# Kernel optimization log

Measured on AMD Instinct MI355X. Metric: run time of the kernel, lower is better.

The kernel has to match this reference:

```python
import jax, jax.numpy as jnp
import numpy as np

N, E, D_IN, D_OUT = 50000, 800000, 128, 64


def setup_inputs() -> dict:
    key = jax.random.key(0)
    ks = jax.random.split(key, 8)
    s = 1.0 / np.sqrt(D_IN)
    return {
        "x": jax.random.normal(ks[0], (N, D_IN), jnp.float32),
        "edge_index": jax.random.randint(ks[1], (2, E), 0, N),
        "edge_weight": jax.random.uniform(ks[2], (E,), jnp.float32),
        "init_w": jax.random.normal(ks[3], (D_IN, D_IN), jnp.float32) * s,
        "gru_w_ih": jax.random.normal(ks[4], (3 * D_IN, D_IN), jnp.float32) * s,
        "gru_w_hh": jax.random.normal(ks[5], (3 * D_IN, D_IN), jnp.float32) * s,
        "gru_b_ih": jnp.zeros((3 * D_IN,), jnp.float32),
        "gru_b_hh": jnp.zeros((3 * D_IN,), jnp.float32),
        "lin_w": jax.random.normal(ks[6], (D_OUT, D_IN), jnp.float32) * s,
        "lin_b": jnp.zeros((D_OUT,), jnp.float32),
    }


def _gru_step(x, h, w_ih, w_hh, b_ih, b_hh):
    # torch GRU gate order: r, z, n
    gi = x @ w_ih.T + b_ih
    gh = h @ w_hh.T + b_hh
    i_r, i_z, i_n = jnp.split(gi, 3, axis=-1)
    h_r, h_z, h_n = jnp.split(gh, 3, axis=-1)
    r = jax.nn.sigmoid(i_r + h_r)
    z = jax.nn.sigmoid(i_z + h_z)
    n = jnp.tanh(i_n + r * h_n)
    return (1.0 - z) * n + z * h


def reference(x, edge_index, edge_weight, init_w, gru_w_ih, gru_w_hh, gru_b_ih, gru_b_hh, lin_w, lin_b):
    n_nodes = x.shape[0]
    # EvolveGCNO: evolve W via one GRU step, W is both input and hidden (rows = GRU batch)
    W = _gru_step(init_w, init_w, gru_w_ih, gru_w_hh, gru_b_ih, gru_b_hh)  # [D_IN, D_IN]

    # gcn_norm with self-loops (fill value 1.0)
    loop = jnp.arange(n_nodes)
    row = jnp.concatenate([edge_index[0], loop])  # source j
    col = jnp.concatenate([edge_index[1], loop])  # target i
    w = jnp.concatenate([edge_weight, jnp.ones((n_nodes,), x.dtype)])
    deg = jax.ops.segment_sum(w, col, num_segments=n_nodes)
    dis = jnp.where(deg > 0, jax.lax.rsqrt(jnp.maximum(deg, 1e-12)), 0.0)
    norm = dis[row] * w * dis[col]  # [E+N]

    xw = x @ W  # [N, D_IN]
    h = jax.ops.segment_sum(norm[:, None] * xw[row], col, num_segments=n_nodes)
    h = jax.nn.relu(h)
    return h @ lin_w.T + lin_b  # [N, D_OUT]
```

## Files before the change

### kernel.cpp

```cpp
#include <hip/hip_runtime.h>
#include <hip/hip_fp16.h>
#include <math.h>

#define NN 50000
#define NE 800000
#define D  128
#define D3 384
#define DO 64
#define NPAD 50048
#define NSH 4

typedef _Float16 f16x2 __attribute__((ext_vector_type(2)));

__device__ __forceinline__ float dot2acc(unsigned int h2bits, unsigned int wbits,
                                         float acc) {
#if __has_builtin(__builtin_amdgcn_fdot2)
  return __builtin_amdgcn_fdot2(__builtin_bit_cast(f16x2, h2bits),
                                __builtin_bit_cast(f16x2, wbits), acc, false);
#else
  float2 hf = __half22float2(__builtin_bit_cast(__half2, h2bits));
  float2 wf = __half22float2(__builtin_bit_cast(__half2, wbits));
  return acc + hf.x * wf.x + hf.y * wf.y;
#endif
}

__device__ __forceinline__ unsigned int pk_f16(float a, float b) {
#if __has_builtin(__builtin_amdgcn_cvt_pkrtz)
  return __builtin_bit_cast(unsigned int, __builtin_amdgcn_cvt_pkrtz(a, b));
#else
  return __builtin_bit_cast(unsigned int, __floats2half2_rn(a, b));
#endif
}

__global__ __launch_bounds__(256) void setup_kernel(
    const float* __restrict__ init_w, const float* __restrict__ w_ih,
    const float* __restrict__ w_hh, const float* __restrict__ b_ih,
    const float* __restrict__ b_hh, __half* __restrict__ Wh,
    unsigned long long* __restrict__ packed4, int* __restrict__ total) {
  if (blockIdx.x >= 64) {
    int i = (blockIdx.x - 64) * 256 + threadIdx.x;
    if (i < NSH * NPAD) packed4[i] = 0ULL;
    if (i == 0) *total = 0;
    return;
  }
  int idx = blockIdx.x * 256 + threadIdx.x;
  int b = idx >> 7;
  int j = idx & 127;
  const float* xr = init_w + b * D;
  const float* wr_i = w_ih + j * D;
  const float* wz_i = w_ih + (D + j) * D;
  const float* wn_i = w_ih + (2 * D + j) * D;
  const float* wr_h = w_hh + j * D;
  const float* wz_h = w_hh + (D + j) * D;
  const float* wn_h = w_hh + (2 * D + j) * D;
  float ir = 0.f, iz = 0.f, in_ = 0.f, hr = 0.f, hz = 0.f, hn = 0.f;
#pragma unroll 4
  for (int k = 0; k < D; ++k) {
    float xv = xr[k];
    ir += xv * wr_i[k];
    iz += xv * wz_i[k];
    in_ += xv * wn_i[k];
    hr += xv * wr_h[k];
    hz += xv * wz_h[k];
    hn += xv * wn_h[k];
  }
  ir += b_ih[j];       hr += b_hh[j];
  iz += b_ih[D + j];   hz += b_hh[D + j];
  in_ += b_ih[2 * D + j]; hn += b_hh[2 * D + j];
  float r = 1.f / (1.f + expf(-(ir + hr)));
  float z = 1.f / (1.f + expf(-(iz + hz)));
  float n = tanhf(in_ + r * hn);
  Wh[idx] = (__half)((1.f - z) * n + z * init_w[idx]);
}

__global__ __launch_bounds__(256) void count_deg_kernel(const int* __restrict__ col,
                                                        const float* __restrict__ ew,
                                                        unsigned long long* __restrict__ packed4,
                                                        int* __restrict__ rank) {
  int e = blockIdx.x * 256 + threadIdx.x;
  if (e < NE) {
    int s = blockIdx.x & (NSH - 1);
    int c = __builtin_nontemporal_load(&col[e]);
    float w = __builtin_nontemporal_load(&ew[e]);
    unsigned long long add = (1ULL << 40) | (unsigned long long)(w * 4294967296.0f);
    unsigned long long old = atomicAdd(&packed4[s * NPAD + c], add);
    __builtin_nontemporal_store((s << 28) | (int)(old >> 40), &rank[e]);
  }
}

__global__ __launch_bounds__(256) void dis_scan_kernel(
    const unsigned long long* __restrict__ packed4, float* __restrict__ dis,
    int* __restrict__ cnt, unsigned int* __restrict__ start4,
    int* __restrict__ total) {
  const unsigned long long M = (1ULL << 40) - 1;
  int i = blockIdx.x * 256 + threadIdx.x;
  int lane = threadIdx.x & 63;
  int c0 = 0, c1 = 0, c2 = 0, c3 = 0;
  float d = 1.0f;
  if (i < NN) {
    unsigned long long p0 = packed4[i];
    unsigned long long p1 = packed4[NPAD + i];
    unsigned long long p2 = packed4[2 * NPAD + i];
    unsigned long long p3 = packed4[3 * NPAD + i];
    c0 = (int)(p0 >> 40);
    c1 = (int)(p1 >> 40);
    c2 = (int)(p2 >> 40);
    c3 = (int)(p3 >> 40);
    unsigned long long dsum = (p0 & M) + (p1 & M) + (p2 & M) + (p3 & M);
    d += (float)dsum * 0x1p-32f;
  }
  int c = c0 + c1 + c2 + c3;
  int cp = (c + 3) & ~3;
  int pre = cp;
#pragma unroll
  for (int off = 1; off < 64; off <<= 1) {
    int t = __shfl_up(pre, off, 64);
    if (lane >= off) pre += t;
  }
  int excl = pre - cp;
  int wtot = __shfl(pre, 63, 64);
  int base = 0;
  if (lane == 63) base = atomicAdd(total, wtot);
  base = __shfl(base, 63, 64);
  if (i < NN) {
    unsigned int st = base + excl;
    start4[i] = st;
    start4[NPAD + i] = st + c0;
    start4[2 * NPAD + i] = st + c0 + c1;
    start4[3 * NPAD + i] = st + c0 + c1 + c2;
    cnt[i] = c;
    dis[i] = rsqrtf(fmaxf(d, 1e-12f));
  }
}

__global__ __launch_bounds__(256) void bucket_kernel(
    const int* __restrict__ row, const int* __restrict__ col,
    const float* __restrict__ ew, const int* __restrict__ rank,
    const float* __restrict__ dis, const unsigned int* __restrict__ start4,
    unsigned int* __restrict__ epack) {
  int e = blockIdx.x * 256 + threadIdx.x;
  if (e >= NE) return;
  int j = __builtin_nontemporal_load(&row[e]);
  int c = __builtin_nontemporal_load(&col[e]);
  float w = __builtin_nontemporal_load(&ew[e]);
  int rk = __builtin_nontemporal_load(&rank[e]);
  int s = rk >> 28;
  int r = rk & 0x0fffffff;
  float nrm = dis[j] * w * dis[c];
  unsigned short wb = __builtin_bit_cast(unsigned short, (_Float16)nrm);
  int slot = start4[s * NPAD + c] + r;
  __builtin_nontemporal_store((unsigned int)j | ((unsigned int)wb << 16),
                              &epack[slot]);
}

__global__ __launch_bounds__(256) void xw_kernel(const float* __restrict__ x,
                                                 const __half* __restrict__ Wh,
                                                 __half* __restrict__ xwh) {
  __shared__ unsigned int U[64 * 128];
  {
    const unsigned short* Wu = (const unsigned short*)Wh;
    for (int i = threadIdx.x; i < 64 * 128; i += 256) {
      int kp = i >> 7, c = i & 127;
      unsigned int lo = Wu[(2 * kp) * D + c];
      unsigned int hi = Wu[(2 * kp + 1) * D + c];
      int sl = (c >> 3) + ((c & 4) ? 16 : 0);
      U[kp * 128 + sl * 4 + (c & 3)] = lo | (hi << 16);
    }
  }
  __syncthreads();
  const int t = threadIdx.x;
  const int rr = t >> 4;
  const int ci = t & 15;
  const uint4* U4 = (const uint4*)U;
  for (int base = blockIdx.x * 32; base < NN; base += gridDim.x * 32) {
    float acc[2][8];
#pragma unroll
    for (int q = 0; q < 2; ++q)
#pragma unroll
      for (int j = 0; j < 8; ++j) acc[q][j] = 0.f;
    const int r0 = base + rr;
    const int r1 = r0 + 16;
    const bool v0 = r0 < NN, v1 = r1 < NN;
    const float* xp0 = x + (long)r0 * D;
    const float* xp1 = x + (long)r1 * D;
#pragma unroll 2
    for (int k0 = 0; k0 < D; k0 += 4) {
      float4 xa = v0 ? *(const float4*)(xp0 + k0) : make_float4(0.f, 0.f, 0.f, 0.f);
      float4 xb = v1 ? *(const float4*)(xp1 + k0) : make_float4(0.f, 0.f, 0.f, 0.f);
      unsigned int xa0 = pk_f16(xa.x, xa.y), xa1 = pk_f16(xa.z, xa.w);
      unsigned int xb0 = pk_f16(xb.x, xb.y), xb1 = pk_f16(xb.z, xb.w);
      int kp = k0 >> 1;
      uint4 wA = U4[kp * 32 + ci];
      uint4 wB = U4[kp * 32 + ci + 16];
      uint4 wC = U4[(kp + 1) * 32 + ci];
      uint4 wD = U4[(kp + 1) * 32 + ci + 16];
      acc[0][0] = dot2acc(xa0, wA.x, acc[0][0]);
      acc[0][1] = dot2acc(xa0, wA.y, acc[0][1]);
      acc[0][2] = dot2acc(xa0, wA.z, acc[0][2]);
      acc[0][3] = dot2acc(xa0, wA.w, acc[0][3]);
      acc[0][4] = dot2acc(xa0, wB.x, acc[0][4]);
      acc[0][5] = dot2acc(xa0, wB.y, acc[0][5]);
      acc[0][6] = dot2acc(xa0, wB.z, acc[0][6]);
      acc[0][7] = dot2acc(xa0, wB.w, acc[0][7]);
      acc[1][0] = dot2acc(xb0, wA.x, acc[1][0]);
      acc[1][1] = dot2acc(xb0, wA.y, acc[1][1]);
      acc[1][2] = dot2acc(xb0, wA.z, acc[1][2]);
      acc[1][3] = dot2acc(xb0, wA.w, acc[1][3]);
      acc[1][4] = dot2acc(xb0, wB.x, acc[1][4]);
      acc[1][5] = dot2acc(xb0, wB.y, acc[1][5]);
      acc[1][6] = dot2acc(xb0, wB.z, acc[1][6]);
      acc[1][7] = dot2acc(xb0, wB.w, acc[1][7]);
      acc[0][0] = dot2acc(xa1, wC.x, acc[0][0]);
      acc[0][1] = dot2acc(xa1, wC.y, acc[0][1]);
      acc[0][2] = dot2acc(xa1, wC.z, acc[0][2]);
      acc[0][3] = dot2acc(xa1, wC.w, acc[0][3]);
      acc[0][4] = dot2acc(xa1, wD.x, acc[0][4]);
      acc[0][5] = dot2acc(xa1, wD.y, acc[0][5]);
      acc[0][6] = dot2acc(xa1, wD.z, acc[0][6]);
      acc[0][7] = dot2acc(xa1, wD.w, acc[0][7]);
      acc[1][0] = dot2acc(xb1, wC.x, acc[1][0]);
      acc[1][1] = dot2acc(xb1, wC.y, acc[1][1]);
      acc[1][2] = dot2acc(xb1, wC.z, acc[1][2]);
      acc[1][3] = dot2acc(xb1, wC.w, acc[1][3]);
      acc[1][4] = dot2acc(xb1, wD.x, acc[1][4]);
      acc[1][5] = dot2acc(xb1, wD.y, acc[1][5]);
      acc[1][6] = dot2acc(xb1, wD.z, acc[1][6]);
      acc[1][7] = dot2acc(xb1, wD.w, acc[1][7]);
    }
#pragma unroll
    for (int q = 0; q < 2; ++q) {
      int r = r0 + q * 16;
      if (r < NN) {
        unsigned int pk[4];
#pragma unroll
        for (int j = 0; j < 4; ++j)
          pk[j] = __builtin_bit_cast(
              unsigned int, __floats2half2_rn(acc[q][2 * j], acc[q][2 * j + 1]));
        *(uint4*)(xwh + (long)r * D + ci * 8) = *(uint4*)pk;
      }
    }
  }
}

__global__ __launch_bounds__(256) void gather_out_kernel(
    const unsigned int* __restrict__ start4, const int* __restrict__ cnt,
    const unsigned int* __restrict__ epack, const float* __restrict__ dis,
    const __half* __restrict__ xwh, const float* __restrict__ lin_w,
    const float* __restrict__ lin_b, float* __restrict__ out) {
  __shared__ unsigned int LTh[64 * 64];
  __shared__ unsigned int hb[4][2][64];
  for (int idx = threadIdx.x; idx < 64 * 64; idx += 256) {
    int kk = idx >> 6, o = idx & 63;
    __half2 w2 = __floats2half2_rn(lin_w[o * D + 2 * kk], lin_w[o * D + 2 * kk + 1]);
    LTh[idx] = __builtin_bit_cast(unsigned int, w2);
  }
  __syncthreads();
  const int wv = threadIdx.x >> 6;
  const int lane = threadIdx.x & 63;
  const float bias = lin_b[lane];
  const __half2* __restrict__ yw2 = (const __half2*)xwh;
  int gw = blockIdx.x * 4 + wv;
  int nw = gridDim.x * 4;
  for (int i = gw; i < NN; i += 2 * nw) {
    const int iB = i + nw;
    const bool hasB = iB < NN;
    float dsA = dis[i], dsA2 = dsA * dsA;
    float2 svA = __half22float2(yw2[(long)i * 64 + lane]);
    float aA0 = dsA2 * svA.x, aA1 = dsA2 * svA.y;
    float aB0 = 0.f, aB1 = 0.f;
    int sA = start4[i], seA = sA + cnt[i];
    int sB = 0, seB = 0;
    if (hasB) {
      float dsB = dis[iB], dsB2 = dsB * dsB;
      float2 svB = __half22float2(yw2[(long)iB * 64 + lane]);
      aB0 = dsB2 * svB.x;
      aB1 = dsB2 * svB.y;
      sB = start4[iB];
      seB = sB + cnt[iB];
    }
    while (sA + 4 <= seA && sB + 4 <= seB) {
      uint4 pA = *(const uint4*)(epack + sA);
      uint4 pB = *(const uint4*)(epack + sB);
      __half2 vA0 = yw2[(long)(pA.x & 0xffff) * 64 + lane];
      __half2 vA1 = yw2[(long)(pA.y & 0xffff) * 64 + lane];
      __half2 vA2 = yw2[(long)(pA.z & 0xffff) * 64 + lane];
      __half2 vA3 = yw2[(long)(pA.w & 0xffff) * 64 + lane];
      __half2 vB0 = yw2[(long)(pB.x & 0xffff) * 64 + lane];
      __half2 vB1 = yw2[(long)(pB.y & 0xffff) * 64 + lane];
      __half2 vB2 = yw2[(long)(pB.z & 0xffff) * 64 + lane];
      __half2 vB3 = yw2[(long)(pB.w & 0xffff) * 64 + lane];
      _Float16 wA0 = __builtin_bit_cast(_Float16, (unsigned short)(pA.x >> 16));
      _Float16 wA1 = __builtin_bit_cast(_Float16, (unsigned short)(pA.y >> 16));
      _Float16 wA2 = __builtin_bit_cast(_Float16, (unsigned short)(pA.z >> 16));
      _Float16 wA3 = __builtin_bit_cast(_Float16, (unsigned short)(pA.w >> 16));
      _Float16 wB0 = __builtin_bit_cast(_Float16, (unsigned short)(pB.x >> 16));
      _Float16 wB1 = __builtin_bit_cast(_Float16, (unsigned short)(pB.y >> 16));
      _Float16 wB2 = __builtin_bit_cast(_Float16, (unsigned short)(pB.z >> 16));
      _Float16 wB3 = __builtin_bit_cast(_Float16, (unsigned short)(pB.w >> 16));
      aA0 += (float)wA0 * (float)__low2half(vA0) + (float)wA1 * (float)__low2half(vA1) +
             (float)wA2 * (float)__low2half(vA2) + (float)wA3 * (float)__low2half(vA3);
      aA1 += (float)wA0 * (float)__high2half(vA0) + (float)wA1 * (float)__high2half(vA1) +
             (float)wA2 * (float)__high2half(vA2) + (float)wA3 * (float)__high2half(vA3);
      aB0 += (float)wB0 * (float)__low2half(vB0) + (float)wB1 * (float)__low2half(vB1) +
             (float)wB2 * (float)__low2half(vB2) + (float)wB3 * (float)__low2half(vB3);
      aB1 += (float)wB0 * (float)__high2half(vB0) + (float)wB1 * (float)__high2half(vB1) +
             (float)wB2 * (float)__high2half(vB2) + (float)wB3 * (float)__high2half(vB3);
      sA += 4;
      sB += 4;
    }
    for (; sA + 4 <= seA; sA += 4) {
      uint4 p = *(const uint4*)(epack + sA);
      __half2 v0 = yw2[(long)(p.x & 0xffff) * 64 + lane];
      __half2 v1 = yw2[(long)(p.y & 0xffff) * 64 + lane];
      __half2 v2 = yw2[(long)(p.z & 0xffff) * 64 + lane];
      __half2 v3 = yw2[(long)(p.w & 0xffff) * 64 + lane];
      _Float16 w0 = __builtin_bit_cast(_Float16, (unsigned short)(p.x >> 16));
      _Float16 w1 = __builtin_bit_cast(_Float16, (unsigned short)(p.y >> 16));
      _Float16 w2 = __builtin_bit_cast(_Float16, (unsigned short)(p.z >> 16));
      _Float16 w3 = __builtin_bit_cast(_Float16, (unsigned short)(p.w >> 16));
      aA0 += (float)w0 * (float)__low2half(v0) + (float)w1 * (float)__low2half(v1) +
             (float)w2 * (float)__low2half(v2) + (float)w3 * (float)__low2half(v3);
      aA1 += (float)w0 * (float)__high2half(v0) + (float)w1 * (float)__high2half(v1) +
             (float)w2 * (float)__high2half(v2) + (float)w3 * (float)__high2half(v3);
    }
    for (; sA < seA; ++sA) {
      unsigned int p = epack[sA];
      _Float16 w0 = __builtin_bit_cast(_Float16, (unsigned short)(p >> 16));
      __half2 v0 = yw2[(long)(p & 0xffff) * 64 + lane];
      aA0 += (float)w0 * (float)__low2half(v0);
      aA1 += (float)w0 * (float)__high2half(v0);
    }
    for (; sB + 4 <= seB; sB += 4) {
      uint4 p = *(const uint4*)(epack + sB);
      __half2 v0 = yw2[(long)(p.x & 0xffff) * 64 + lane];
      __half2 v1 = yw2[(long)(p.y & 0xffff) * 64 + lane];
      __half2 v2 = yw2[(long)(p.z & 0xffff) * 64 + lane];
      __half2 v3 = yw2[(long)(p.w & 0xffff) * 64 + lane];
      _Float16 w0 = __builtin_bit_cast(_Float16, (unsigned short)(p.x >> 16));
      _Float16 w1 = __builtin_bit_cast(_Float16, (unsigned short)(p.y >> 16));
      _Float16 w2 = __builtin_bit_cast(_Float16, (unsigned short)(p.z >> 16));
      _Float16 w3 = __builtin_bit_cast(_Float16, (unsigned short)(p.w >> 16));
      aB0 += (float)w0 * (float)__low2half(v0) + (float)w1 * (float)__low2half(v1) +
             (float)w2 * (float)__low2half(v2) + (float)w3 * (float)__low2half(v3);
      aB1 += (float)w0 * (float)__high2half(v0) + (float)w1 * (float)__high2half(v1) +
             (float)w2 * (float)__high2half(v2) + (float)w3 * (float)__high2half(v3);
    }
    for (; sB < seB; ++sB) {
      unsigned int p = epack[sB];
      _Float16 w0 = __builtin_bit_cast(_Float16, (unsigned short)(p >> 16));
      __half2 v0 = yw2[(long)(p & 0xffff) * 64 + lane];
      aB0 += (float)w0 * (float)__low2half(v0);
      aB1 += (float)w0 * (float)__high2half(v0);
    }
    hb[wv][0][lane] = __builtin_bit_cast(
        unsigned int, __floats2half2_rn(fmaxf(aA0, 0.f), fmaxf(aA1, 0.f)));
    if (hasB) {
      hb[wv][1][lane] = __builtin_bit_cast(
          unsigned int, __floats2half2_rn(fmaxf(aB0, 0.f), fmaxf(aB1, 0.f)));
    }
    asm volatile("s_waitcnt lgkmcnt(0)" ::: "memory");
    {
      float ac0 = bias, ac1 = 0.f, ac2 = 0.f, ac3 = 0.f;
      const uint4* hrow = (const uint4*)&hb[wv][0][0];
#pragma unroll
      for (int c = 0; c < 16; ++c) {
        uint4 v = hrow[c];
        ac0 = dot2acc(v.x, LTh[(4 * c + 0) * 64 + lane], ac0);
        ac1 = dot2acc(v.y, LTh[(4 * c + 1) * 64 + lane], ac1);
        ac2 = dot2acc(v.z, LTh[(4 * c + 2) * 64 + lane], ac2);
        ac3 = dot2acc(v.w, LTh[(4 * c + 3) * 64 + lane], ac3);
      }
      __builtin_nontemporal_store((ac0 + ac1) + (ac2 + ac3),
                                  &out[(long)i * DO + lane]);
    }
    if (hasB) {
      float ac0 = bias, ac1 = 0.f, ac2 = 0.f, ac3 = 0.f;
      const uint4* hrow = (const uint4*)&hb[wv][1][0];
#pragma unroll
      for (int c = 0; c < 16; ++c) {
        uint4 v = hrow[c];
        ac0 = dot2acc(v.x, LTh[(4 * c + 0) * 64 + lane], ac0);
        ac1 = dot2acc(v.y, LTh[(4 * c + 1) * 64 + lane], ac1);
        ac2 = dot2acc(v.z, LTh[(4 * c + 2) * 64 + lane], ac2);
        ac3 = dot2acc(v.w, LTh[(4 * c + 3) * 64 + lane], ac3);
      }
      __builtin_nontemporal_store((ac0 + ac1) + (ac2 + ac3),
                                  &out[(long)iB * DO + lane]);
    }
    asm volatile("s_waitcnt lgkmcnt(0)" ::: "memory");
  }
}

extern "C" void kernel_launch(void* const* d_in, const int* in_sizes, int n_in,
                              void* d_out, int out_size, void* d_ws, size_t ws_size,
                              hipStream_t stream) {
  const float* x      = (const float*)d_in[0];
  const int*   eidx   = (const int*)d_in[1];
  const float* ew     = (const float*)d_in[2];
  const float* init_w = (const float*)d_in[3];
  const float* w_ih   = (const float*)d_in[4];
  const float* w_hh   = (const float*)d_in[5];
  const float* b_ih   = (const float*)d_in[6];
  const float* b_hh   = (const float*)d_in[7];
  const float* lin_w  = (const float*)d_in[8];
  const float* lin_b  = (const float*)d_in[9];
  float* out = (float*)d_out;
  const int* row = eidx;
  const int* col = eidx + NE;

  float* ws    = (float*)d_ws;
  __half* Wh   = (__half*)ws;
  unsigned long long* packed4 = (unsigned long long*)(ws + 8192);
  float* dis   = (float*)(packed4 + NSH * NPAD);
  int*   cnt   = (int*)(dis + NPAD);
  unsigned int* strt4 = (unsigned int*)(cnt + NPAD);
  int*   total = (int*)(strt4 + NSH * NPAD);
  int*   rank  = total + 64;
  unsigned int* epack = (unsigned int*)(rank + NE);
  __half* xwh  = (__half*)(epack + 1000064);

  setup_kernel<<<64 + (NSH * NPAD + 255) / 256, 256, 0, stream>>>(
      init_w, w_ih, w_hh, b_ih, b_hh, Wh, packed4, total);
  count_deg_kernel<<<(NE + 255) / 256, 256, 0, stream>>>(col, ew, packed4, rank);
  dis_scan_kernel<<<(NN + 255) / 256, 256, 0, stream>>>(packed4, dis, cnt, strt4,
                                                        total);
  bucket_kernel<<<(NE + 255) / 256, 256, 0, stream>>>(row, col, ew, rank, dis, strt4,
                                                      epack);
  xw_kernel<<<1563, 256, 0, stream>>>(x, Wh, xwh);
  gather_out_kernel<<<2048, 256, 0, stream>>>(strt4, cnt, epack, dis, xwh,
                                              lin_w, lin_b, out);
}
```

Baseline: 189.2 us.

## Fuse degree counting with x@W into one launch, read prepacked W from global

The setup kernel now writes W in fp16 already interleaved as k-pairs per output column, so the xw stage reads it straight from global/L2 instead of staging and swizzling it through shared memory. The degree-count atomics and the x@W matmul are merged into one kernel launch with disjoint block ranges, so the atomic-heavy and compute-heavy work can overlap and one launch is dropped. Node segments are now padded to multiples of 8, and the gather loop gains an 8-edge unrolled path for more loads in flight, at the cost of a larger epack buffer and more padding. Reading W from global rather than LDS may add cache traffic in the matmul inner loop.

```diff
diff --git a/kernel.cpp b/kernel.cpp
--- a/kernel.cpp
+++ b/kernel.cpp
@@ -9,6 +9,8 @@
 #define DO 64
 #define NPAD 50048
 #define NSH 4
+#define CD_BLOCKS 3125
+#define XW_BLOCKS 1563
 
 typedef _Float16 f16x2 __attribute__((ext_vector_type(2)));
 
@@ -35,7 +37,7 @@
 __global__ __launch_bounds__(256) void setup_kernel(
     const float* __restrict__ init_w, const float* __restrict__ w_ih,
     const float* __restrict__ w_hh, const float* __restrict__ b_ih,
-    const float* __restrict__ b_hh, __half* __restrict__ Wh,
+    const float* __restrict__ b_hh, __half* __restrict__ Whp,
     unsigned long long* __restrict__ packed4, int* __restrict__ total) {
   if (blockIdx.x >= 64) {
     int i = (blockIdx.x - 64) * 256 + threadIdx.x;
@@ -70,109 +72,33 @@
   float r = 1.f / (1.f + expf(-(ir + hr)));
   float z = 1.f / (1.f + expf(-(iz + hz)));
   float n = tanhf(in_ + r * hn);
-  Wh[idx] = (__half)((1.f - z) * n + z * init_w[idx]);
-}
-
-__global__ __launch_bounds__(256) void count_deg_kernel(const int* __restrict__ col,
-                                                        const float* __restrict__ ew,
-                                                        unsigned long long* __restrict__ packed4,
-                                                        int* __restrict__ rank) {
-  int e = blockIdx.x * 256 + threadIdx.x;
-  if (e < NE) {
-    int s = blockIdx.x & (NSH - 1);
-    int c = __builtin_nontemporal_load(&col[e]);
-    float w = __builtin_nontemporal_load(&ew[e]);
-    unsigned long long add = (1ULL << 40) | (unsigned long long)(w * 4294967296.0f);
-    unsigned long long old = atomicAdd(&packed4[s * NPAD + c], add);
-    __builtin_nontemporal_store((s << 28) | (int)(old >> 40), &rank[e]);
-  }
-}
-
-__global__ __launch_bounds__(256) void dis_scan_kernel(
-    const unsigned long long* __restrict__ packed4, float* __restrict__ dis,
-    int* __restrict__ cnt, unsigned int* __restrict__ start4,
-    int* __restrict__ total) {
-  const unsigned long long M = (1ULL << 40) - 1;
-  int i = blockIdx.x * 256 + threadIdx.x;
-  int lane = threadIdx.x & 63;
-  int c0 = 0, c1 = 0, c2 = 0, c3 = 0;
-  float d = 1.0f;
-  if (i < NN) {
-    unsigned long long p0 = packed4[i];
-    unsigned long long p1 = packed4[NPAD + i];
-    unsigned long long p2 = packed4[2 * NPAD + i];
-    unsigned long long p3 = packed4[3 * NPAD + i];
-    c0 = (int)(p0 >> 40);
-    c1 = (int)(p1 >> 40);
-    c2 = (int)(p2 >> 40);
-    c3 = (int)(p3 >> 40);
-    unsigned long long dsum = (p0 & M) + (p1 & M) + (p2 & M) + (p3 & M);
-    d += (float)dsum * 0x1p-32f;
-  }
-  int c = c0 + c1 + c2 + c3;
-  int cp = (c + 3) & ~3;
-  int pre = cp;
-#pragma unroll
-  for (int off = 1; off < 64; off <<= 1) {
-    int t = __shfl_up(pre, off, 64);
-    if (lane >= off) pre += t;
-  }
-  int excl = pre - cp;
-  int wtot = __shfl(pre, 63, 64);
-  int base = 0;
-  if (lane == 63) base = atomicAdd(total, wtot);
-  base = __shfl(base, 63, 64);
-  if (i < NN) {
-    unsigned int st = base + excl;
-    start4[i] = st;
-    start4[NPAD + i] = st + c0;
-    start4[2 * NPAD + i] = st + c0 + c1;
-    start4[3 * NPAD + i] = st + c0 + c1 + c2;
-    cnt[i] = c;
-    dis[i] = rsqrtf(fmaxf(d, 1e-12f));
-  }
-}
-
-__global__ __launch_bounds__(256) void bucket_kernel(
-    const int* __restrict__ row, const int* __restrict__ col,
-    const float* __restrict__ ew, const int* __restrict__ rank,
-    const float* __restrict__ dis, const unsigned int* __restrict__ start4,
-    unsigned int* __restrict__ epack) {
-  int e = blockIdx.x * 256 + threadIdx.x;
-  if (e >= NE) return;
-  int j = __builtin_nontemporal_load(&row[e]);
-  int c = __builtin_nontemporal_load(&col[e]);
-  float w = __builtin_nontemporal_load(&ew[e]);
-  int rk = __builtin_nontemporal_load(&rank[e]);
-  int s = rk >> 28;
-  int r = rk & 0x0fffffff;
-  float nrm = dis[j] * w * dis[c];
-  unsigned short wb = __builtin_bit_cast(unsigned short, (_Float16)nrm);
-  int slot = start4[s * NPAD + c] + r;
-  __builtin_nontemporal_store((unsigned int)j | ((unsigned int)wb << 16),
-                              &epack[slot]);
-}
-
-__global__ __launch_bounds__(256) void xw_kernel(const float* __restrict__ x,
-                                                 const __half* __restrict__ Wh,
-                                                 __half* __restrict__ xwh) {
-  __shared__ unsigned int U[64 * 128];
-  {
-    const unsigned short* Wu = (const unsigned short*)Wh;
-    for (int i = threadIdx.x; i < 64 * 128; i += 256) {
-      int kp = i >> 7, c = i & 127;
-      unsigned int lo = Wu[(2 * kp) * D + c];
-      unsigned int hi = Wu[(2 * kp + 1) * D + c];
-      int sl = (c >> 3) + ((c & 4) ? 16 : 0);
-      U[kp * 128 + sl * 4 + (c & 3)] = lo | (hi << 16);
-    }
-  }
-  __syncthreads();
+  float w = (1.f - z) * n + z * init_w[idx];
+  Whp[(b >> 1) * 256 + j * 2 + (b & 1)] = (__half)w;
+}
+
+__global__ __launch_bounds__(256) void cdxw_kernel(
+    const float* __restrict__ x, const __half* __restrict__ Whp,
+    const int* __restrict__ col, const float* __restrict__ ew,
+    unsigned long long* __restrict__ packed4, int* __restrict__ rank,
+    __half* __restrict__ xwh) {
+  if (blockIdx.x < CD_BLOCKS) {
+    int e = blockIdx.x * 256 + threadIdx.x;
+    if (e < NE) {
+      int s = blockIdx.x & (NSH - 1);
+      int c = __builtin_nontemporal_load(&col[e]);
+      float w = __builtin_nontemporal_load(&ew[e]);
+      unsigned long long add = (1ULL << 40) | (unsigned long long)(w * 4294967296.0f);
+      unsigned long long old = atomicAdd(&packed4[s * NPAD + c], add);
+      __builtin_nontemporal_store((s << 28) | (int)(old >> 40), &rank[e]);
+    }
+    return;
+  }
   const int t = threadIdx.x;
   const int rr = t >> 4;
   const int ci = t & 15;
-  const uint4* U4 = (const uint4*)U;
-  for (int base = blockIdx.x * 32; base < NN; base += gridDim.x * 32) {
+  const uint4* __restrict__ U4 = (const uint4*)Whp;
+  const int xb = blockIdx.x - CD_BLOCKS;
+  for (int base = xb * 32; base < NN; base += XW_BLOCKS * 32) {
     float acc[2][8];
 #pragma unroll
     for (int q = 0; q < 2; ++q)
@@ -186,14 +112,14 @@
 #pragma unroll 2
     for (int k0 = 0; k0 < D; k0 += 4) {
       float4 xa = v0 ? *(const float4*)(xp0 + k0) : make_float4(0.f, 0.f, 0.f, 0.f);
-      float4 xb = v1 ? *(const float4*)(xp1 + k0) : make_float4(0.f, 0.f, 0.f, 0.f);
+      float4 xb4 = v1 ? *(const float4*)(xp1 + k0) : make_float4(0.f, 0.f, 0.f, 0.f);
       unsigned int xa0 = pk_f16(xa.x, xa.y), xa1 = pk_f16(xa.z, xa.w);
-      unsigned int xb0 = pk_f16(xb.x, xb.y), xb1 = pk_f16(xb.z, xb.w);
+      unsigned int xb0 = pk_f16(xb4.x, xb4.y), xb1 = pk_f16(xb4.z, xb4.w);
       int kp = k0 >> 1;
-      uint4 wA = U4[kp * 32 + ci];
-      uint4 wB = U4[kp * 32 + ci + 16];
-      uint4 wC = U4[(kp + 1) * 32 + ci];
-      uint4 wD = U4[(kp + 1) * 32 + ci + 16];
+      uint4 wA = U4[kp * 32 + 2 * ci];
+      uint4 wB = U4[kp * 32 + 2 * ci + 1];
+      uint4 wC = U4[(kp + 1) * 32 + 2 * ci];
+      uint4 wD = U4[(kp + 1) * 32 + 2 * ci + 1];
       acc[0][0] = dot2acc(xa0, wA.x, acc[0][0]);
       acc[0][1] = dot2acc(xa0, wA.y, acc[0][1]);
       acc[0][2] = dot2acc(xa0, wA.z, acc[0][2]);
@@ -242,6 +168,99 @@
   }
 }
 
+__global__ __launch_bounds__(256) void dis_scan_kernel(
+    const unsigned long long* __restrict__ packed4, float* __restrict__ dis,
+    int* __restrict__ cnt, unsigned int* __restrict__ start4,
+    int* __restrict__ total) {
+  const unsigned long long M = (1ULL << 40) - 1;
+  int i = blockIdx.x * 256 + threadIdx.x;
+  int lane = threadIdx.x & 63;
+  int c0 = 0, c1 = 0, c2 = 0, c3 = 0;
+  float d = 1.0f;
+  if (i < NN) {
+    unsigned long long p0 = packed4[i];
+    unsigned long long p1 = packed4[NPAD + i];
+    unsigned long long p2 = packed4[2 * NPAD + i];
+    unsigned long long p3 = packed4[3 * NPAD + i];
+    c0 = (int)(p0 >> 40);
+    c1 = (int)(p1 >> 40);
+    c2 = (int)(p2 >> 40);
+    c3 = (int)(p3 >> 40);
+    unsigned long long dsum = (p0 & M) + (p1 & M) + (p2 & M) + (p3 & M);
+    d += (float)dsum * 0x1p-32f;
+  }
+  int c = c0 + c1 + c2 + c3;
+  int cp = (c + 7) & ~7;
+  int pre = cp;
+#pragma unroll
+  for (int off = 1; off < 64; off <<= 1) {
+    int t = __shfl_up(pre, off, 64);
+    if (lane >= off) pre += t;
+  }
+  int excl = pre - cp;
+  int wtot = __shfl(pre, 63, 64);
+  int base = 0;
+  if (lane == 63) base = atomicAdd(total, wtot);
+  base = __shfl(base, 63, 64);
+  if (i < NN) {
+    unsigned int st = base + excl;
+    start4[i] = st;
+    start4[NPAD + i] = st + c0;
+    start4[2 * NPAD + i] = st + c0 + c1;
+    start4[3 * NPAD + i] = st + c0 + c1 + c2;
+    cnt[i] = c;
+    dis[i] = rsqrtf(fmaxf(d, 1e-12f));
+  }
+}
+
+__global__ __launch_bounds__(256) void bucket_kernel(
+    const int* __restrict__ row, const int* __restrict__ col,
+    const float* __restrict__ ew, const int* __restrict__ rank,
+    const float* __restrict__ dis, const unsigned int* __restrict__ start4,
+    unsigned int* __restrict__ epack) {
+  int e = blockIdx.x * 256 + threadIdx.x;
+  if (e >= NE) return;
+  int j = __builtin_nontemporal_load(&row[e]);
+  int c = __builtin_nontemporal_load(&col[e]);
+  float w = __builtin_nontemporal_load(&ew[e]);
+  int rk = __builtin_nontemporal_load(&rank[e]);
+  int s = rk >> 28;
+  int r = rk & 0x0fffffff;
+  float nrm = dis[j] * w * dis[c];
+  unsigned short wb = __builtin_bit_cast(unsigned short, (_Float16)nrm);
+  int slot = start4[s * NPAD + c] + r;
+  __builtin_nontemporal_store((unsigned int)j | ((unsigned int)wb << 16),
+                              &epack[slot]);
+}
+
+#define EDGE4(p_, a0_, a1_)                                                     \
+  {                                                                             \
+    __half2 v0_ = yw2[(long)(p_.x & 0xffff) * 64 + lane];                       \
+    __half2 v1_ = yw2[(long)(p_.y & 0xffff) * 64 + lane];                       \
+    __half2 v2_ = yw2[(long)(p_.z & 0xffff) * 64 + lane];                       \
+    __half2 v3_ = yw2[(long)(p_.w & 0xffff) * 64 + lane];                       \
+    _Float16 w0_ = __builtin_bit_cast(_Float16, (unsigned short)(p_.x >> 16));  \
+    _Float16 w1_ = __builtin_bit_cast(_Float16, (unsigned short)(p_.y >> 16));  \
+    _Float16 w2_ = __builtin_bit_cast(_Float16, (unsigned short)(p_.z >> 16));  \
+    _Float16 w3_ = __builtin_bit_cast(_Float16, (unsigned short)(p_.w >> 16));  \
+    a0_ += (float)w0_ * (float)__low2half(v0_) +                                \
+           (float)w1_ * (float)__low2half(v1_) +                                \
+           (float)w2_ * (float)__low2half(v2_) +                                \
+           (float)w3_ * (float)__low2half(v3_);                                 \
+    a1_ += (float)w0_ * (float)__high2half(v0_) +                               \
+           (float)w1_ * (float)__high2half(v1_) +                               \
+           (float)w2_ * (float)__high2half(v2_) +                               \
+           (float)w3_ * (float)__high2half(v3_);                                \
+  }
+#define EDGE1(s_, a0_, a1_)                                                     \
+  {                                                                             \
+    unsigned int p_ = epack[s_];                                                \
+    _Float16 w0_ = __builtin_bit_cast(_Float16, (unsigned short)(p_ >> 16));    \
+    __half2 v0_ = yw2[(long)(p_ & 0xffff) * 64 + lane];                         \
+    a0_ += (float)w0_ * (float)__low2half(v0_);                                 \
+    a1_ += (float)w0_ * (float)__high2half(v0_);                                \
+  }
+
 __global__ __launch_bounds__(256) void gather_out_kernel(
     const unsigned int* __restrict__ start4, const int* __restrict__ cnt,
     const unsigned int* __restrict__ epack, const float* __restrict__ dis,
@@ -278,80 +297,36 @@
       sB = start4[iB];
       seB = sB + cnt[iB];
     }
+    while (sA + 8 <= seA && sB + 8 <= seB) {
+      uint4 pA0 = *(const uint4*)(epack + sA);
+      uint4 pA1 = *(const uint4*)(epack + sA + 4);
+      uint4 pB0 = *(const uint4*)(epack + sB);
+      uint4 pB1 = *(const uint4*)(epack + sB + 4);
+      EDGE4(pA0, aA0, aA1);
+      EDGE4(pA1, aA0, aA1);
+      EDGE4(pB0, aB0, aB1);
+      EDGE4(pB1, aB0, aB1);
+      sA += 8;
+      sB += 8;
+    }
     while (sA + 4 <= seA && sB + 4 <= seB) {
       uint4 pA = *(const uint4*)(epack + sA);
       uint4 pB = *(const uint4*)(epack + sB);
-      __half2 vA0 = yw2[(long)(pA.x & 0xffff) * 64 + lane];
-      __half2 vA1 = yw2[(long)(pA.y & 0xffff) * 64 + lane];
-      __half2 vA2 = yw2[(long)(pA.z & 0xffff) * 64 + lane];
-      __half2 vA3 = yw2[(long)(pA.w & 0xffff) * 64 + lane];
-      __half2 vB0 = yw2[(long)(pB.x & 0xffff) * 64 + lane];
-      __half2 vB1 = yw2[(long)(pB.y & 0xffff) * 64 + lane];
-      __half2 vB2 = yw2[(long)(pB.z & 0xffff) * 64 + lane];
-      __half2 vB3 = yw2[(long)(pB.w & 0xffff) * 64 + lane];
-      _Float16 wA0 = __builtin_bit_cast(_Float16, (unsigned short)(pA.x >> 16));
-      _Float16 wA1 = __builtin_bit_cast(_Float16, (unsigned short)(pA.y >> 16));
-      _Float16 wA2 = __builtin_bit_cast(_Float16, (unsigned short)(pA.z >> 16));
-      _Float16 wA3 = __builtin_bit_cast(_Float16, (unsigned short)(pA.w >> 16));
-      _Float16 wB0 = __builtin_bit_cast(_Float16, (unsigned short)(pB.x >> 16));
-      _Float16 wB1 = __builtin_bit_cast(_Float16, (unsigned short)(pB.y >> 16));
-      _Float16 wB2 = __builtin_bit_cast(_Float16, (unsigned short)(pB.z >> 16));
-      _Float16 wB3 = __builtin_bit_cast(_Float16, (unsigned short)(pB.w >> 16));
-      aA0 += (float)wA0 * (float)__low2half(vA0) + (float)wA1 * (float)__low2half(vA1) +
-             (float)wA2 * (float)__low2half(vA2) + (float)wA3 * (float)__low2half(vA3);
-      aA1 += (float)wA0 * (float)__high2half(vA0) + (float)wA1 * (float)__high2half(vA1) +
-             (float)wA2 * (float)__high2half(vA2) + (float)wA3 * (float)__high2half(vA3);
-      aB0 += (float)wB0 * (float)__low2half(vB0) + (float)wB1 * (float)__low2half(vB1) +
-             (float)wB2 * (float)__low2half(vB2) + (float)wB3 * (float)__low2half(vB3);
-      aB1 += (float)wB0 * (float)__high2half(vB0) + (float)wB1 * (float)__high2half(vB1) +
-             (float)wB2 * (float)__high2half(vB2) + (float)wB3 * (float)__high2half(vB3);
+      EDGE4(pA, aA0, aA1);
+      EDGE4(pB, aB0, aB1);
       sA += 4;
       sB += 4;
     }
     for (; sA + 4 <= seA; sA += 4) {
       uint4 p = *(const uint4*)(epack + sA);
-      __half2 v0 = yw2[(long)(p.x & 0xffff) * 64 + lane];
-      __half2 v1 = yw2[(long)(p.y & 0xffff) * 64 + lane];
-      __half2 v2 = yw2[(long)(p.z & 0xffff) * 64 + lane];
-      __half2 v3 = yw2[(long)(p.w & 0xffff) * 64 + lane];
-      _Float16 w0 = __builtin_bit_cast(_Float16, (unsigned short)(p.x >> 16));
-      _Float16 w1 = __builtin_bit_cast(_Float16, (unsigned short)(p.y >> 16));
-      _Float16 w2 = __builtin_bit_cast(_Float16, (unsigned short)(p.z >> 16));
-      _Float16 w3 = __builtin_bit_cast(_Float16, (unsigned short)(p.w >> 16));
-      aA0 += (float)w0 * (float)__low2half(v0) + (float)w1 * (float)__low2half(v1) +
-             (float)w2 * (float)__low2half(v2) + (float)w3 * (float)__low2half(v3);
-      aA1 += (float)w0 * (float)__high2half(v0) + (float)w1 * (float)__high2half(v1) +
-             (float)w2 * (float)__high2half(v2) + (float)w3 * (float)__high2half(v3);
-    }
-    for (; sA < seA; ++sA) {
-      unsigned int p = epack[sA];
-      _Float16 w0 = __builtin_bit_cast(_Float16, (unsigned short)(p >> 16));
-      __half2 v0 = yw2[(long)(p & 0xffff) * 64 + lane];
-      aA0 += (float)w0 * (float)__low2half(v0);
-      aA1 += (float)w0 * (float)__high2half(v0);
-    }
+      EDGE4(p, aA0, aA1);
+    }
+    for (; sA < seA; ++sA) EDGE1(sA, aA0, aA1);
     for (; sB + 4 <= seB; sB += 4) {
       uint4 p = *(const uint4*)(epack + sB);
-      __half2 v0 = yw2[(long)(p.x & 0xffff) * 64 + lane];
-      __half2 v1 = yw2[(long)(p.y & 0xffff) * 64 + lane];
-      __half2 v2 = yw2[(long)(p.z & 0xffff) * 64 + lane];
-      __half2 v3 = yw2[(long)(p.w & 0xffff) * 64 + lane];
-      _Float16 w0 = __builtin_bit_cast(_Float16, (unsigned short)(p.x >> 16));
-      _Float16 w1 = __builtin_bit_cast(_Float16, (unsigned short)(p.y >> 16));
-      _Float16 w2 = __builtin_bit_cast(_Float16, (unsigned short)(p.z >> 16));
-      _Float16 w3 = __builtin_bit_cast(_Float16, (unsigned short)(p.w >> 16));
-      aB0 += (float)w0 * (float)__low2half(v0) + (float)w1 * (float)__low2half(v1) +
-             (float)w2 * (float)__low2half(v2) + (float)w3 * (float)__low2half(v3);
-      aB1 += (float)w0 * (float)__high2half(v0) + (float)w1 * (float)__high2half(v1) +
-             (float)w2 * (float)__high2half(v2) + (float)w3 * (float)__high2half(v3);
-    }
-    for (; sB < seB; ++sB) {
-      unsigned int p = epack[sB];
-      _Float16 w0 = __builtin_bit_cast(_Float16, (unsigned short)(p >> 16));
-      __half2 v0 = yw2[(long)(p & 0xffff) * 64 + lane];
-      aB0 += (float)w0 * (float)__low2half(v0);
-      aB1 += (float)w0 * (float)__high2half(v0);
-    }
+      EDGE4(p, aB0, aB1);
+    }
+    for (; sB < seB; ++sB) EDGE1(sB, aB0, aB1);
     hb[wv][0][lane] = __builtin_bit_cast(
         unsigned int, __floats2half2_rn(fmaxf(aA0, 0.f), fmaxf(aA1, 0.f)));
     if (hasB) {
@@ -409,7 +384,7 @@
   const int* col = eidx + NE;
 
   float* ws    = (float*)d_ws;
-  __half* Wh   = (__half*)ws;
+  __half* Whp  = (__half*)ws;
   unsigned long long* packed4 = (unsigned long long*)(ws + 8192);
   float* dis   = (float*)(packed4 + NSH * NPAD);
   int*   cnt   = (int*)(dis + NPAD);
@@ -417,16 +392,16 @@
   int*   total = (int*)(strt4 + NSH * NPAD);
   int*   rank  = total + 64;
   unsigned int* epack = (unsigned int*)(rank + NE);
-  __half* xwh  = (__half*)(epack + 1000064);
+  __half* xwh  = (__half*)(epack + 1200128);
 
   setup_kernel<<<64 + (NSH * NPAD + 255) / 256, 256, 0, stream>>>(
-      init_w, w_ih, w_hh, b_ih, b_hh, Wh, packed4, total);
-  count_deg_kernel<<<(NE + 255) / 256, 256, 0, stream>>>(col, ew, packed4, rank);
+      init_w, w_ih, w_hh, b_ih, b_hh, Whp, packed4, total);
+  cdxw_kernel<<<CD_BLOCKS + XW_BLOCKS, 256, 0, stream>>>(x, Whp, col, ew, packed4,
+                                                         rank, xwh);
   dis_scan_kernel<<<(NN + 255) / 256, 256, 0, stream>>>(packed4, dis, cnt, strt4,
                                                         total);
   bucket_kernel<<<(NE + 255) / 256, 256, 0, stream>>>(row, col, ew, rank, dis, strt4,
                                                       epack);
-  xw_kernel<<<1563, 256, 0, stream>>>(x, Wh, xwh);
   gather_out_kernel<<<2048, 256, 0, stream>>>(strt4, cnt, epack, dis, xwh,
                                               lin_w, lin_b, out);
 }
```

Measured after the change: 210.9 us. 1.11x slower.
